# Kernel optimization log

Measured on AMD Instinct MI355X. Metric: run time of the kernel, lower is better.

Reference implementation:

```python
import jax, jax.numpy as jnp
import numpy as np

B, T, IN, H = 256, 512, 19, 512  # batch, seq_len, input_size, hidden_size
OUT = 1


def setup_inputs() -> dict:
    key = jax.random.key(0)
    ks = jax.random.split(key, 16)
    std = 1.0 / np.sqrt(H)  # reset_parameters: uniform(-1/sqrt(H), 1/sqrt(H))
    u = lambda k, shape: jax.random.uniform(k, shape, jnp.float32, -std, std)
    return {
        "input": jax.random.normal(ks[0], (B, T, IN), jnp.float32),
        "l1_Wx": u(ks[1], (4 * H, IN)),
        "l1_bx": u(ks[2], (4 * H,)),
        "l1_Wh": u(ks[3], (4 * H, H)),
        "l1_bh": u(ks[4], (4 * H,)),
        "l2_Wx": u(ks[5], (4 * H, H)),
        "l2_bx": u(ks[6], (4 * H,)),
        "l2_Wh": u(ks[7], (4 * H, H)),
        "l2_bh": u(ks[8], (4 * H,)),
        "fc1_W": u(ks[9], (H // 2, H)),
        "fc1_b": u(ks[10], (H // 2,)),
        "fc2_W": u(ks[11], (H // 4, H // 2)),
        "fc2_b": u(ks[12], (H // 4,)),
        "fc3_W": u(ks[13], (OUT, H // 4)),
        "fc3_b": u(ks[14], (OUT,)),
    }


def _lstm_layer(x, Wx, bx, Wh, bh):
    # Precompute the input projection for all timesteps (identical math to
    # per-step xh(input), but one big GEMM). x: [B, T, in] -> pre: [B, T, 4H]
    pre = jnp.einsum('bti,gi->btg', x, Wx) + bx
    h_dim = Wh.shape[1]

    def step(carry, p_t):
        h, c = carry
        gates = p_t + h @ Wh.T + bh  # [B, 4H]
        i, f, g, o = jnp.split(gates, 4, axis=-1)
        c = jax.nn.sigmoid(f) * c + jax.nn.sigmoid(i) * jnp.tanh(g)
        h = jax.nn.sigmoid(o) * jnp.tanh(c)
        return (h, c), h

    h0 = jnp.zeros((x.shape[0], h_dim), x.dtype)
    _, hs = jax.lax.scan(step, (h0, h0), jnp.swapaxes(pre, 0, 1))  # hs: [T, B, H]
    return jnp.swapaxes(hs, 0, 1)  # [B, T, H]


def reference(input, l1_Wx, l1_bx, l1_Wh, l1_bh, l2_Wx, l2_bx, l2_Wh, l2_bh,
              fc1_W, fc1_b, fc2_W, fc2_b, fc3_W, fc3_b):
    h1 = _lstm_layer(input, l1_Wx, l1_bx, l1_Wh, l1_bh)
    h2 = _lstm_layer(h1, l2_Wx, l2_bx, l2_Wh, l2_bh)
    out = h2[:, -1, :]  # last timestep of top layer
    out = jax.nn.relu(out @ fc1_W.T + fc1_b)  # dropout = identity (inference)
    out = jax.nn.relu(out @ fc2_W.T + fc2_b)
    out = out @ fc3_W.T + fc3_b
    return jnp.squeeze(out)  # [B]
```

## Files before the change

### kernel.cpp

```cpp
#include <hip/hip_runtime.h>
#include <hip/hip_cooperative_groups.h>

namespace cg = cooperative_groups;

#define Bb   256
#define Tt   512
#define INx  19
#define Hh   512
#define NWG  256
#define NTHR 512

typedef unsigned int u32;
typedef unsigned long long u64;

__device__ __forceinline__ float sigf(float x) { return 1.0f / (1.0f + __expf(-x)); }
__device__ __forceinline__ float tanhfast(float x) {
    float e = __expf(2.0f * x);
    return 1.0f - 2.0f / (e + 1.0f);
}

union pcast { u64 u; float2 f; };
__device__ __forceinline__ void gstore2(float2* p, float2 v) {
    pcast c; c.f = v;
    __hip_atomic_store((u64*)p, c.u, __ATOMIC_RELAXED, __HIP_MEMORY_SCOPE_AGENT);
}

__device__ __forceinline__ void gbar(u32* flags, int wgid, int tid, u32 phase) {
    __syncthreads();
    if (tid == 0)
        __hip_atomic_store(&flags[wgid], phase, __ATOMIC_RELEASE, __HIP_MEMORY_SCOPE_AGENT);
    if (tid < NWG) {
        const u32* fp = &flags[tid];
        while (__hip_atomic_load(fp, __ATOMIC_RELAXED, __HIP_MEMORY_SCOPE_AGENT) < phase)
            __builtin_amdgcn_s_sleep(2);
    }
    __syncthreads();
    __builtin_amdgcn_fence(__ATOMIC_ACQUIRE, "agent");
}

__device__ __forceinline__ void ldh(const float4* __restrict__ hp, int c,
                                    float4 (&A)[4], float4 (&B)[4]) {
    #pragma unroll
    for (int kk = 0; kk < 4; ++kk) {
        A[kk] = hp[(size_t)(c * 4 + kk) * 128];
        B[kk] = hp[(size_t)(c * 4 + kk) * 128 + 1];
    }
}

__device__ __forceinline__ void fmac(const float4 (&A)[4], const float4 (&B)[4],
                                     const float* __restrict__ wk,
                                     float (&a1)[4][4], float (&ax)[4][4], float (&ah)[4][4]) {
    #pragma unroll
    for (int g = 0; g < 4; ++g) {
        const float4 w1 = *reinterpret_cast<const float4*>(wk + (0 + g) * 528);
        const float4 w2 = *reinterpret_cast<const float4*>(wk + (4 + g) * 528);
        const float4 w3 = *reinterpret_cast<const float4*>(wk + (8 + g) * 528);
        a1[g][0] += A[0].x*w1.x + A[1].x*w1.y + A[2].x*w1.z + A[3].x*w1.w;
        a1[g][1] += A[0].z*w1.x + A[1].z*w1.y + A[2].z*w1.z + A[3].z*w1.w;
        a1[g][2] += B[0].x*w1.x + B[1].x*w1.y + B[2].x*w1.z + B[3].x*w1.w;
        a1[g][3] += B[0].z*w1.x + B[1].z*w1.y + B[2].z*w1.z + B[3].z*w1.w;
        ax[g][0] += A[0].x*w2.x + A[1].x*w2.y + A[2].x*w2.z + A[3].x*w2.w;
        ax[g][1] += A[0].z*w2.x + A[1].z*w2.y + A[2].z*w2.z + A[3].z*w2.w;
        ax[g][2] += B[0].x*w2.x + B[1].x*w2.y + B[2].x*w2.z + B[3].x*w2.w;
        ax[g][3] += B[0].z*w2.x + B[1].z*w2.y + B[2].z*w2.z + B[3].z*w2.w;
        ah[g][0] += A[0].y*w3.x + A[1].y*w3.y + A[2].y*w3.z + A[3].y*w3.w;
        ah[g][1] += A[0].w*w3.x + A[1].w*w3.y + A[2].w*w3.z + A[3].w*w3.w;
        ah[g][2] += B[0].y*w3.x + B[1].y*w3.y + B[2].y*w3.z + B[3].y*w3.w;
        ah[g][3] += B[0].w*w3.x + B[1].w*w3.y + B[2].w*w3.z + B[3].w*w3.w;
    }
}

__global__ void __launch_bounds__(NTHR, 2)
lstm_fused(const float* __restrict__ input,
           const float* __restrict__ l1_Wx, const float* __restrict__ l1_bx,
           const float* __restrict__ l1_Wh, const float* __restrict__ l1_bh,
           const float* __restrict__ l2_Wx, const float* __restrict__ l2_bx,
           const float* __restrict__ l2_Wh, const float* __restrict__ l2_bh,
           const float* __restrict__ fc1_W, const float* __restrict__ fc1_b,
           const float* __restrict__ fc2_W, const float* __restrict__ fc2_b,
           const float* __restrict__ fc3_W, const float* __restrict__ fc3_b,
           float* __restrict__ out, float* __restrict__ ws)
{
    __shared__ float wlds[24 * 528];
    __shared__ float wx1l[8 * 20];
    __shared__ float fcb[Hh + 256 + 128];

    cg::grid_group grid = cg::this_grid();
    const int wgid = blockIdx.x;
    const int jb = wgid * 2;
    const int tid = threadIdx.x;
    const int wid = tid >> 6, lane = tid & 63;
    const int su = wid & 1;
    const int bh = wid >> 1;
    const int kq = lane >> 4;
    const int bg = lane & 15;
    const int bB = bh * 64 + bg * 4;
    const int j  = jb + su;

    float2* PA = (float2*)ws;
    float2* PB = PA + Hh * Bb;
    u32* flags = (u32*)(PB + Hh * Bb);

    if (tid == 0)
        __hip_atomic_store(&flags[wgid], 0u, __ATOMIC_RELAXED, __HIP_MEMORY_SCOPE_AGENT);
    grid.sync();

    for (int idx = tid; idx < 24 * 512; idx += NTHR) {
        const int row = idx >> 9, k = idx & 511;
        const int sru = row >= 12 ? 1 : 0;
        const int rr = row - sru * 12;
        const int m = rr >> 2, g = rr & 3;
        const float* src = (m == 0) ? l1_Wh : (m == 1) ? l2_Wx : l2_Wh;
        wlds[row * 528 + (k >> 7) * 132 + (k & 127)] =
            src[(size_t)(g * Hh + jb + sru) * Hh + k];
    }
    if (tid < 8 * INx) {
        const int r = tid / INx, i = tid - r * INx;
        const int sru = r >> 2, g = r & 3;
        wx1l[r * 20 + i] = l1_Wx[(size_t)(g * Hh + jb + sru) * INx + i];
    }
    float b1r[4], b2r[4];
    #pragma unroll
    for (int g = 0; g < 4; ++g) {
        const int row = g * Hh + j;
        b1r[g] = l1_bx[row] + l1_bh[row];
        b2r[g] = l2_bx[row] + l2_bh[row];
    }
    __syncthreads();

    float c1[4], c2[4];
    #pragma unroll
    for (int b = 0; b < 4; ++b) {
        const float* xr = input + (size_t)(bB + b) * Tt * INx;
        float s[4];
        #pragma unroll
        for (int g = 0; g < 4; ++g) {
            float acc = b1r[g];
            #pragma unroll
            for (int i = 0; i < INx; ++i) acc += xr[i] * wx1l[(su * 4 + g) * 20 + i];
            s[g] = acc;
        }
        c1[b] = sigf(s[0]) * tanhfast(s[2]);
        c2[b] = 0.0f;
        const float h1v = sigf(s[3]) * tanhfast(c1[b]);
        if (kq == 0) gstore2(&PA[(size_t)j * Bb + bB + b], make_float2(h1v, 0.0f));
    }
    gbar(flags, wgid, tid, 1u);

    const float2* Pc = PA; float2* Pn = PB;
    const float* wlane = wlds + su * (12 * 528) + kq * 132;

    for (int t = 0; t < Tt; ++t) {
        const bool doL1 = (t < Tt - 1);

        float a1[4][4], ax[4][4], ah[4][4];
        #pragma unroll
        for (int g = 0; g < 4; ++g)
            #pragma unroll
            for (int b = 0; b < 4; ++b) { a1[g][b] = 0.f; ax[g][b] = 0.f; ah[g][b] = 0.f; }

        const float4* hp = (const float4*)Pc + (size_t)(kq * 128) * 128 + (bB >> 1);

        float4 Ac[4], Bc[4], An[4], Bn[4];
        ldh(hp, 0, Ac, Bc);
        #pragma unroll 1
        for (int c = 0; c < 32; c += 2) {
            ldh(hp, c + 1, An, Bn);
            fmac(Ac, Bc, wlane + c * 4, a1, ax, ah);
            if (c < 30) ldh(hp, c + 2, Ac, Bc);
            fmac(An, Bn, wlane + (c + 1) * 4, a1, ax, ah);
        }

        #pragma unroll
        for (int g = 0; g < 4; ++g) {
            #pragma unroll
            for (int b = 0; b < 4; ++b) {
                float v = a1[g][b]; v += __shfl_xor(v, 16, 64); v += __shfl_xor(v, 32, 64); a1[g][b] = v;
                float w = ax[g][b]; w += __shfl_xor(w, 16, 64); w += __shfl_xor(w, 32, 64); ax[g][b] = w;
                float u = ah[g][b]; u += __shfl_xor(u, 16, 64); u += __shfl_xor(u, 32, 64); ah[g][b] = u;
            }
        }

        #pragma unroll
        for (int b = 0; b < 4; ++b) {
            float s2[4];
            #pragma unroll
            for (int g = 0; g < 4; ++g) s2[g] = ax[g][b] + ah[g][b] + b2r[g];

            float h1v = 0.0f;
            if (doL1) {
                const float* xr = input + ((size_t)(bB + b) * Tt + (t + 1)) * INx;
                float s1[4];
                #pragma unroll
                for (int g = 0; g < 4; ++g) {
                    float acc = a1[g][b] + b1r[g];
                    #pragma unroll
                    for (int i = 0; i < INx; ++i) acc += xr[i] * wx1l[(su * 4 + g) * 20 + i];
                    s1[g] = acc;
                }
                const float ig = sigf(s1[0]), fg = sigf(s1[1]);
                const float gg = tanhfast(s1[2]), og = sigf(s1[3]);
                c1[b] = fg * c1[b] + ig * gg;
                h1v = og * tanhfast(c1[b]);
            }
            const float ig = sigf(s2[0]), fg = sigf(s2[1]);
            const float gg = tanhfast(s2[2]), og = sigf(s2[3]);
            c2[b] = fg * c2[b] + ig * gg;
            const float h2v = og * tanhfast(c2[b]);
            if (kq == 0) gstore2(&Pn[(size_t)j * Bb + bB + b], make_float2(h1v, h2v));
        }

        gbar(flags, wgid, tid, (u32)(t + 2));

        const float2* tp = Pc; Pc = Pn; Pn = (float2*)tp;
    }

    float* hh  = fcb;
    float* a1s = fcb + Hh;
    float* a2s = fcb + Hh + 256;
    hh[tid] = Pc[(size_t)tid * Bb + wgid].y;
    __syncthreads();
    if (tid < 256) {
        float acc = fc1_b[tid];
        const float* wr = fc1_W + (size_t)tid * Hh;
        for (int i = 0; i < Hh; ++i) acc += wr[i] * hh[i];
        a1s[tid] = fmaxf(acc, 0.0f);
    }
    __syncthreads();
    if (tid < 128) {
        float acc = fc2_b[tid];
        const float* wr = fc2_W + (size_t)tid * 256;
        for (int i = 0; i < 256; ++i) acc += wr[i] * a1s[i];
        a2s[tid] = fmaxf(acc, 0.0f);
    }
    __syncthreads();
    if (tid == 0) {
        float acc = fc3_b[0];
        for (int i = 0; i < 128; ++i) acc += fc3_W[i] * a2s[i];
        out[wgid] = acc;
    }
}

extern "C" void kernel_launch(void* const* d_in, const int* in_sizes, int n_in,
                              void* d_out, int out_size, void* d_ws, size_t ws_size,
                              hipStream_t stream)
{
    (void)in_sizes; (void)n_in; (void)out_size; (void)ws_size;

    const float* input = (const float*)d_in[0];
    const float* l1_Wx = (const float*)d_in[1];
    const float* l1_bx = (const float*)d_in[2];
    const float* l1_Wh = (const float*)d_in[3];
    const float* l1_bh = (const float*)d_in[4];
    const float* l2_Wx = (const float*)d_in[5];
    const float* l2_bx = (const float*)d_in[6];
    const float* l2_Wh = (const float*)d_in[7];
    const float* l2_bh = (const float*)d_in[8];
    const float* fc1_W = (const float*)d_in[9];
    const float* fc1_b = (const float*)d_in[10];
    const float* fc2_W = (const float*)d_in[11];
    const float* fc2_b = (const float*)d_in[12];
    const float* fc3_W = (const float*)d_in[13];
    const float* fc3_b = (const float*)d_in[14];
    float* out = (float*)d_out;
    float* ws  = (float*)d_ws;

    void* args[] = {
        &input,
        &l1_Wx, &l1_bx, &l1_Wh, &l1_bh,
        &l2_Wx, &l2_bx, &l2_Wh, &l2_bh,
        &fc1_W, &fc1_b, &fc2_W, &fc2_b, &fc3_W, &fc3_b,
        &out, &ws
    };
    hipLaunchCooperativeKernel((void*)lstm_fused, dim3(NWG), dim3(NTHR), args, 0, stream);
}
```

Baseline: 30.44 ms.

## Read LSTM weights from global memory and reduce K-split partials through LDS

Stops staging the per-workgroup weight rows in LDS. Each wave now reads its weight slices straight from global memory (wave-uniform addresses, cached), and the work is repartitioned so each wave covers a K quarter for all 64 batch groups. The cross-lane shuffle reduction is replaced by writing partial sums to an LDS buffer, followed by a __syncthreads, after which every thread owns one (unit, batch) cell to finish the gate math. This removes the serial per-thread loop over 4 batches and the redundant kq lanes in the epilogue, at the cost of global or cache weight traffic on every timestep plus an extra block barrier.

After: 29.86 ms. No clear change (-1.9%).

```diff
diff --git a/kernel.cpp b/kernel.cpp
--- a/kernel.cpp
+++ b/kernel.cpp
@@ -10,6 +10,12 @@
 #define NWG  256
 #define NTHR 512
 
+#define PART_FLOATS (8 * 12 * 256)
+#define WX1_FLOATS  (8 * 20)
+#define FCB_FLOATS  (Hh + 256 + 128)
+#define SMEM_FLOATS (PART_FLOATS + WX1_FLOATS + FCB_FLOATS)
+#define SMEM_BYTES  (SMEM_FLOATS * 4)
+
 typedef unsigned int u32;
 typedef unsigned long long u64;
 
@@ -48,13 +54,15 @@
 }
 
 __device__ __forceinline__ void fmac(const float4 (&A)[4], const float4 (&B)[4],
-                                     const float* __restrict__ wk,
+                                     const float* const (&wb1)[4],
+                                     const float* const (&wb2)[4],
+                                     const float* const (&wb3)[4], int c4,
                                      float (&a1)[4][4], float (&ax)[4][4], float (&ah)[4][4]) {
     #pragma unroll
     for (int g = 0; g < 4; ++g) {
-        const float4 w1 = *reinterpret_cast<const float4*>(wk + (0 + g) * 528);
-        const float4 w2 = *reinterpret_cast<const float4*>(wk + (4 + g) * 528);
-        const float4 w3 = *reinterpret_cast<const float4*>(wk + (8 + g) * 528);
+        const float4 w1 = *reinterpret_cast<const float4*>(wb1[g] + c4);
+        const float4 w2 = *reinterpret_cast<const float4*>(wb2[g] + c4);
+        const float4 w3 = *reinterpret_cast<const float4*>(wb3[g] + c4);
         a1[g][0] += A[0].x*w1.x + A[1].x*w1.y + A[2].x*w1.z + A[3].x*w1.w;
         a1[g][1] += A[0].z*w1.x + A[1].z*w1.y + A[2].z*w1.z + A[3].z*w1.w;
         a1[g][2] += B[0].x*w1.x + B[1].x*w1.y + B[2].x*w1.z + B[3].x*w1.w;
@@ -81,21 +89,23 @@
            const float* __restrict__ fc3_W, const float* __restrict__ fc3_b,
            float* __restrict__ out, float* __restrict__ ws)
 {
-    __shared__ float wlds[24 * 528];
-    __shared__ float wx1l[8 * 20];
-    __shared__ float fcb[Hh + 256 + 128];
+    extern __shared__ float smem[];
+    float* part = smem;
+    float* wx1l = smem + PART_FLOATS;
+    float* fcb  = wx1l + WX1_FLOATS;
 
     cg::grid_group grid = cg::this_grid();
     const int wgid = blockIdx.x;
     const int jb = wgid * 2;
     const int tid = threadIdx.x;
-    const int wid = tid >> 6, lane = tid & 63;
-    const int su = wid & 1;
-    const int bh = wid >> 1;
-    const int kq = lane >> 4;
-    const int bg = lane & 15;
-    const int bB = bh * 64 + bg * 4;
-    const int j  = jb + su;
+
+    const int wu = __builtin_amdgcn_readfirstlane(tid >> 6);
+    const int su = wu & 1;
+    const int kq = wu >> 1;
+    const int bg = tid & 63;
+    const int su2 = tid >> 8;
+    const int fb  = tid & 255;
+    const int j2  = jb + su2;
 
     float2* PA = (float2*)ws;
     float2* PB = PA + Hh * Bb;
@@ -105,50 +115,50 @@
         __hip_atomic_store(&flags[wgid], 0u, __ATOMIC_RELAXED, __HIP_MEMORY_SCOPE_AGENT);
     grid.sync();
 
-    for (int idx = tid; idx < 24 * 512; idx += NTHR) {
-        const int row = idx >> 9, k = idx & 511;
-        const int sru = row >= 12 ? 1 : 0;
-        const int rr = row - sru * 12;
-        const int m = rr >> 2, g = rr & 3;
-        const float* src = (m == 0) ? l1_Wh : (m == 1) ? l2_Wx : l2_Wh;
-        wlds[row * 528 + (k >> 7) * 132 + (k & 127)] =
-            src[(size_t)(g * Hh + jb + sru) * Hh + k];
-    }
+    const float* wb1[4]; const float* wb2[4]; const float* wb3[4];
+    {
+        const int j = jb + su;
+        #pragma unroll
+        for (int g = 0; g < 4; ++g) {
+            const size_t off = (size_t)(g * Hh + j) * Hh + kq * 128;
+            wb1[g] = l1_Wh + off;
+            wb2[g] = l2_Wx + off;
+            wb3[g] = l2_Wh + off;
+        }
+    }
+
     if (tid < 8 * INx) {
         const int r = tid / INx, i = tid - r * INx;
-        const int sru = r >> 2, g = r & 3;
-        wx1l[r * 20 + i] = l1_Wx[(size_t)(g * Hh + jb + sru) * INx + i];
+        const int u = r >> 2, g = r & 3;
+        wx1l[r * 20 + i] = l1_Wx[(size_t)(g * Hh + jb + u) * INx + i];
     }
     float b1r[4], b2r[4];
     #pragma unroll
     for (int g = 0; g < 4; ++g) {
-        const int row = g * Hh + j;
+        const int row = g * Hh + j2;
         b1r[g] = l1_bx[row] + l1_bh[row];
         b2r[g] = l2_bx[row] + l2_bh[row];
     }
     __syncthreads();
 
-    float c1[4], c2[4];
-    #pragma unroll
-    for (int b = 0; b < 4; ++b) {
-        const float* xr = input + (size_t)(bB + b) * Tt * INx;
+    float c1 = 0.f, c2 = 0.f;
+    {
+        const float* xr = input + (size_t)fb * Tt * INx;
         float s[4];
         #pragma unroll
         for (int g = 0; g < 4; ++g) {
             float acc = b1r[g];
             #pragma unroll
-            for (int i = 0; i < INx; ++i) acc += xr[i] * wx1l[(su * 4 + g) * 20 + i];
+            for (int i = 0; i < INx; ++i) acc += xr[i] * wx1l[(su2 * 4 + g) * 20 + i];
             s[g] = acc;
         }
-        c1[b] = sigf(s[0]) * tanhfast(s[2]);
-        c2[b] = 0.0f;
-        const float h1v = sigf(s[3]) * tanhfast(c1[b]);
-        if (kq == 0) gstore2(&PA[(size_t)j * Bb + bB + b], make_float2(h1v, 0.0f));
+        c1 = sigf(s[0]) * tanhfast(s[2]);
+        gstore2(&PA[(size_t)j2 * Bb + fb], make_float2(sigf(s[3]) * tanhfast(c1), 0.f));
     }
     gbar(flags, wgid, tid, 1u);
 
     const float2* Pc = PA; float2* Pn = PB;
-    const float* wlane = wlds + su * (12 * 528) + kq * 132;
+    const int blk = su * 4 + kq;
 
     for (int t = 0; t < Tt; ++t) {
         const bool doL1 = (t < Tt - 1);
@@ -159,55 +169,63 @@
             #pragma unroll
             for (int b = 0; b < 4; ++b) { a1[g][b] = 0.f; ax[g][b] = 0.f; ah[g][b] = 0.f; }
 
-        const float4* hp = (const float4*)Pc + (size_t)(kq * 128) * 128 + (bB >> 1);
-
-        float4 Ac[4], Bc[4], An[4], Bn[4];
-        ldh(hp, 0, Ac, Bc);
+        const float4* hp = (const float4*)Pc + (size_t)(kq * 128) * 128 + bg * 2;
+
+        float4 E0[4], E1[4], O0[4], O1[4];
+        ldh(hp, 0, E0, E1);
         #pragma unroll 1
         for (int c = 0; c < 32; c += 2) {
-            ldh(hp, c + 1, An, Bn);
-            fmac(Ac, Bc, wlane + c * 4, a1, ax, ah);
-            if (c < 30) ldh(hp, c + 2, Ac, Bc);
-            fmac(An, Bn, wlane + (c + 1) * 4, a1, ax, ah);
-        }
-
-        #pragma unroll
-        for (int g = 0; g < 4; ++g) {
-            #pragma unroll
-            for (int b = 0; b < 4; ++b) {
-                float v = a1[g][b]; v += __shfl_xor(v, 16, 64); v += __shfl_xor(v, 32, 64); a1[g][b] = v;
-                float w = ax[g][b]; w += __shfl_xor(w, 16, 64); w += __shfl_xor(w, 32, 64); ax[g][b] = w;
-                float u = ah[g][b]; u += __shfl_xor(u, 16, 64); u += __shfl_xor(u, 32, 64); ah[g][b] = u;
+            ldh(hp, c + 1, O0, O1);
+            fmac(E0, E1, wb1, wb2, wb3, (c    ) * 4, a1, ax, ah);
+            if (c < 30) ldh(hp, c + 2, E0, E1);
+            fmac(O0, O1, wb1, wb2, wb3, (c + 1) * 4, a1, ax, ah);
+        }
+
+        {
+            float* pw = part + (size_t)(blk * 12) * 256 + bg * 4;
+            #pragma unroll
+            for (int g = 0; g < 4; ++g) {
+                *reinterpret_cast<float4*>(pw + (0 + g) * 256) = make_float4(a1[g][0], a1[g][1], a1[g][2], a1[g][3]);
+                *reinterpret_cast<float4*>(pw + (4 + g) * 256) = make_float4(ax[g][0], ax[g][1], ax[g][2], ax[g][3]);
+                *reinterpret_cast<float4*>(pw + (8 + g) * 256) = make_float4(ah[g][0], ah[g][1], ah[g][2], ah[g][3]);
             }
         }
-
-        #pragma unroll
-        for (int b = 0; b < 4; ++b) {
-            float s2[4];
-            #pragma unroll
-            for (int g = 0; g < 4; ++g) s2[g] = ax[g][b] + ah[g][b] + b2r[g];
-
-            float h1v = 0.0f;
+        __syncthreads();
+
+        {
+            float s1[4], s2[4];
+            #pragma unroll
+            for (int g = 0; g < 4; ++g) {
+                float A1 = 0.f, AX = 0.f, AH = 0.f;
+                #pragma unroll
+                for (int q = 0; q < 4; ++q) {
+                    const float* pr = part + (size_t)((su2 * 4 + q) * 12) * 256 + fb;
+                    A1 += pr[(0 + g) * 256];
+                    AX += pr[(4 + g) * 256];
+                    AH += pr[(8 + g) * 256];
+                }
+                s1[g] = A1 + b1r[g];
+                s2[g] = AX + AH + b2r[g];
+            }
+            float h1v = 0.f;
             if (doL1) {
-                const float* xr = input + ((size_t)(bB + b) * Tt + (t + 1)) * INx;
-                float s1[4];
+                const float* xr = input + ((size_t)fb * Tt + t + 1) * INx;
                 #pragma unroll
                 for (int g = 0; g < 4; ++g) {
-                    float acc = a1[g][b] + b1r[g];
+                    float acc = s1[g];
                     #pragma unroll
-                    for (int i = 0; i < INx; ++i) acc += xr[i] * wx1l[(su * 4 + g) * 20 + i];
+                    for (int i = 0; i < INx; ++i) acc += xr[i] * wx1l[(su2 * 4 + g) * 20 + i];
                     s1[g] = acc;
                 }
                 const float ig = sigf(s1[0]), fg = sigf(s1[1]);
                 const float gg = tanhfast(s1[2]), og = sigf(s1[3]);
-                c1[b] = fg * c1[b] + ig * gg;
-                h1v = og * tanhfast(c1[b]);
+                c1 = fg * c1 + ig * gg;
+                h1v = og * tanhfast(c1);
             }
             const float ig = sigf(s2[0]), fg = sigf(s2[1]);
             const float gg = tanhfast(s2[2]), og = sigf(s2[3]);
-            c2[b] = fg * c2[b] + ig * gg;
-            const float h2v = og * tanhfast(c2[b]);
-            if (kq == 0) gstore2(&Pn[(size_t)j * Bb + bB + b], make_float2(h1v, h2v));
+            c2 = fg * c2 + ig * gg;
+            gstore2(&Pn[(size_t)j2 * Bb + fb], make_float2(h1v, og * tanhfast(c2)));
         }
 
         gbar(flags, wgid, tid, (u32)(t + 2));
@@ -265,6 +283,9 @@
     float* out = (float*)d_out;
     float* ws  = (float*)d_ws;
 
+    hipFuncSetAttribute((const void*)lstm_fused,
+                        hipFuncAttributeMaxDynamicSharedMemorySize, SMEM_BYTES);
+
     void* args[] = {
         &input,
         &l1_Wx, &l1_bx, &l1_Wh, &l1_bh,
@@ -272,5 +293,6 @@
         &fc1_W, &fc1_b, &fc2_W, &fc2_b, &fc3_W, &fc3_b,
         &out, &ws
     };
-    hipLaunchCooperativeKernel((void*)lstm_fused, dim3(NWG), dim3(NTHR), args, 0, stream);
-}
+    hipLaunchCooperativeKernel((void*)lstm_fused, dim3(NWG), dim3(NTHR), args,
+                               SMEM_BYTES, stream);
+}
```

## Replace workgroup grid barrier with per-wave batch-slice barriers and remap lanes

Applied to the files above, without the earlier changes.

Replaces the whole-grid barrier (syncthreads plus a flag spin) with per-wavefront barriers. Each wave owns a 32-batch slice across all workgroups and syncs only with the matching wave in other blocks, using a separate flag array per slice. Lanes are remapped so one wave covers both hidden units over a batch slice with 4 k-quarters, and the layer-2 Wx/Wh accumulators are merged. It also drops the explicit software prefetch of h and pads the LDS stride to 544. The aim is to cut barrier latency and coupling between waves, at the cost of 8x more flag traffic and the loss of load/compute overlap.

Result: slower. 40.71 ms (+33.7%).

```diff
diff --git a/kernel.cpp b/kernel.cpp
--- a/kernel.cpp
+++ b/kernel.cpp
@@ -25,50 +25,24 @@
     __hip_atomic_store((u64*)p, c.u, __ATOMIC_RELAXED, __HIP_MEMORY_SCOPE_AGENT);
 }
 
-__device__ __forceinline__ void gbar(u32* flags, int wgid, int tid, u32 phase) {
-    __syncthreads();
-    if (tid == 0)
-        __hip_atomic_store(&flags[wgid], phase, __ATOMIC_RELEASE, __HIP_MEMORY_SCOPE_AGENT);
-    if (tid < NWG) {
-        const u32* fp = &flags[tid];
-        while (__hip_atomic_load(fp, __ATOMIC_RELAXED, __HIP_MEMORY_SCOPE_AGENT) < phase)
-            __builtin_amdgcn_s_sleep(2);
-    }
-    __syncthreads();
+__device__ __forceinline__ void wbar(u32* fS, int wgid, int lane, u32 phase) {
+    asm volatile("s_waitcnt vmcnt(0)" ::: "memory");
+    if (lane == 0)
+        __hip_atomic_store(&fS[wgid], phase, __ATOMIC_RELEASE, __HIP_MEMORY_SCOPE_AGENT);
+    const u32* f = fS + lane;
+    for (;;) {
+        bool d = (__hip_atomic_load(f,       __ATOMIC_RELAXED, __HIP_MEMORY_SCOPE_AGENT) >= phase)
+              && (__hip_atomic_load(f + 64,  __ATOMIC_RELAXED, __HIP_MEMORY_SCOPE_AGENT) >= phase)
+              && (__hip_atomic_load(f + 128, __ATOMIC_RELAXED, __HIP_MEMORY_SCOPE_AGENT) >= phase)
+              && (__hip_atomic_load(f + 192, __ATOMIC_RELAXED, __HIP_MEMORY_SCOPE_AGENT) >= phase);
+        if (__all(d)) break;
+        __builtin_amdgcn_s_sleep(2);
+    }
     __builtin_amdgcn_fence(__ATOMIC_ACQUIRE, "agent");
 }
 
-__device__ __forceinline__ void ldh(const float4* __restrict__ hp, int c,
-                                    float4 (&A)[4], float4 (&B)[4]) {
-    #pragma unroll
-    for (int kk = 0; kk < 4; ++kk) {
-        A[kk] = hp[(size_t)(c * 4 + kk) * 128];
-        B[kk] = hp[(size_t)(c * 4 + kk) * 128 + 1];
-    }
-}
-
-__device__ __forceinline__ void fmac(const float4 (&A)[4], const float4 (&B)[4],
-                                     const float* __restrict__ wk,
-                                     float (&a1)[4][4], float (&ax)[4][4], float (&ah)[4][4]) {
-    #pragma unroll
-    for (int g = 0; g < 4; ++g) {
-        const float4 w1 = *reinterpret_cast<const float4*>(wk + (0 + g) * 528);
-        const float4 w2 = *reinterpret_cast<const float4*>(wk + (4 + g) * 528);
-        const float4 w3 = *reinterpret_cast<const float4*>(wk + (8 + g) * 528);
-        a1[g][0] += A[0].x*w1.x + A[1].x*w1.y + A[2].x*w1.z + A[3].x*w1.w;
-        a1[g][1] += A[0].z*w1.x + A[1].z*w1.y + A[2].z*w1.z + A[3].z*w1.w;
-        a1[g][2] += B[0].x*w1.x + B[1].x*w1.y + B[2].x*w1.z + B[3].x*w1.w;
-        a1[g][3] += B[0].z*w1.x + B[1].z*w1.y + B[2].z*w1.z + B[3].z*w1.w;
-        ax[g][0] += A[0].x*w2.x + A[1].x*w2.y + A[2].x*w2.z + A[3].x*w2.w;
-        ax[g][1] += A[0].z*w2.x + A[1].z*w2.y + A[2].z*w2.z + A[3].z*w2.w;
-        ax[g][2] += B[0].x*w2.x + B[1].x*w2.y + B[2].x*w2.z + B[3].x*w2.w;
-        ax[g][3] += B[0].z*w2.x + B[1].z*w2.y + B[2].z*w2.z + B[3].z*w2.w;
-        ah[g][0] += A[0].y*w3.x + A[1].y*w3.y + A[2].y*w3.z + A[3].y*w3.w;
-        ah[g][1] += A[0].w*w3.x + A[1].w*w3.y + A[2].w*w3.z + A[3].w*w3.w;
-        ah[g][2] += B[0].y*w3.x + B[1].y*w3.y + B[2].y*w3.z + B[3].y*w3.w;
-        ah[g][3] += B[0].w*w3.x + B[1].w*w3.y + B[2].w*w3.z + B[3].w*w3.w;
-    }
-}
+#define WROWS 24
+#define WSTR  544
 
 __global__ void __launch_bounds__(NTHR, 2)
 lstm_fused(const float* __restrict__ input,
@@ -81,7 +55,7 @@
            const float* __restrict__ fc3_W, const float* __restrict__ fc3_b,
            float* __restrict__ out, float* __restrict__ ws)
 {
-    __shared__ float wlds[24 * 528];
+    __shared__ float wlds[WROWS * WSTR];
     __shared__ float wx1l[8 * 20];
     __shared__ float fcb[Hh + 256 + 128];
 
@@ -89,35 +63,37 @@
     const int wgid = blockIdx.x;
     const int jb = wgid * 2;
     const int tid = threadIdx.x;
-    const int wid = tid >> 6, lane = tid & 63;
-    const int su = wid & 1;
-    const int bh = wid >> 1;
-    const int kq = lane >> 4;
-    const int bg = lane & 15;
-    const int bB = bh * 64 + bg * 4;
-    const int j  = jb + su;
+
+    const int sid  = __builtin_amdgcn_readfirstlane(tid >> 6);
+    const int lane = tid & 63;
+    const int u    = lane >> 5;
+    const int kq   = (lane >> 3) & 3;
+    const int bp   = lane & 7;
+    const int b0   = sid * 32 + bp * 4;
+    const int j    = jb + u;
 
     float2* PA = (float2*)ws;
-    float2* PB = PA + Hh * Bb;
-    u32* flags = (u32*)(PB + Hh * Bb);
-
-    if (tid == 0)
-        __hip_atomic_store(&flags[wgid], 0u, __ATOMIC_RELAXED, __HIP_MEMORY_SCOPE_AGENT);
+    float2* PB = PA + (size_t)Hh * Bb;
+    u32* flags = (u32*)(PB + (size_t)Hh * Bb);
+    u32* fS = flags + sid * 256;
+
+    if (tid < 8)
+        __hip_atomic_store(&flags[tid * 256 + wgid], 0u,
+                           __ATOMIC_RELAXED, __HIP_MEMORY_SCOPE_AGENT);
     grid.sync();
 
-    for (int idx = tid; idx < 24 * 512; idx += NTHR) {
-        const int row = idx >> 9, k = idx & 511;
-        const int sru = row >= 12 ? 1 : 0;
-        const int rr = row - sru * 12;
+    for (int idx = tid; idx < WROWS * Hh; idx += NTHR) {
+        const int ri = idx >> 9, k = idx & 511;
+        const int uu = ri / 12, rr = ri - uu * 12;
         const int m = rr >> 2, g = rr & 3;
         const float* src = (m == 0) ? l1_Wh : (m == 1) ? l2_Wx : l2_Wh;
-        wlds[row * 528 + (k >> 7) * 132 + (k & 127)] =
-            src[(size_t)(g * Hh + jb + sru) * Hh + k];
+        wlds[ri * WSTR + (k >> 7) * 136 + (k & 127)] =
+            src[(size_t)(g * Hh + jb + uu) * Hh + k];
     }
     if (tid < 8 * INx) {
         const int r = tid / INx, i = tid - r * INx;
-        const int sru = r >> 2, g = r & 3;
-        wx1l[r * 20 + i] = l1_Wx[(size_t)(g * Hh + jb + sru) * INx + i];
+        const int uu = r >> 2, g = r & 3;
+        wx1l[r * 20 + i] = l1_Wx[(size_t)(g * Hh + jb + uu) * INx + i];
     }
     float b1r[4], b2r[4];
     #pragma unroll
@@ -130,90 +106,114 @@
 
     float c1[4], c2[4];
     #pragma unroll
-    for (int b = 0; b < 4; ++b) {
-        const float* xr = input + (size_t)(bB + b) * Tt * INx;
-        float s[4];
+    for (int b = 0; b < 4; ++b) { c1[b] = 0.f; c2[b] = 0.f; }
+    if (kq == 0) {
+        #pragma unroll
+        for (int b = 0; b < 4; ++b) {
+            const float* xr = input + (size_t)(b0 + b) * Tt * INx;
+            float s[4];
+            #pragma unroll
+            for (int g = 0; g < 4; ++g) {
+                float acc = b1r[g];
+                #pragma unroll
+                for (int i = 0; i < INx; ++i) acc += xr[i] * wx1l[(u * 4 + g) * 20 + i];
+                s[g] = acc;
+            }
+            c1[b] = sigf(s[0]) * tanhfast(s[2]);
+            gstore2(&PA[(size_t)j * Bb + b0 + b],
+                    make_float2(sigf(s[3]) * tanhfast(c1[b]), 0.f));
+        }
+    }
+    wbar(fS, wgid, lane, 1u);
+
+    const float2* Pc = PA; float2* Pn = PB;
+    const float* wk0 = wlds + (u * 12) * WSTR + kq * 136;
+
+    for (int t = 0; t < Tt; ++t) {
+        const bool doL1 = (t < Tt - 1);
+
+        float a1[4][4], a2[4][4];
+        #pragma unroll
+        for (int g = 0; g < 4; ++g)
+            #pragma unroll
+            for (int b = 0; b < 4; ++b) { a1[g][b] = 0.f; a2[g][b] = 0.f; }
+
+        const float4* hp = (const float4*)Pc + (size_t)(kq * 128) * 128 + (b0 >> 1);
+
+        #pragma unroll 1
+        for (int c = 0; c < 32; ++c) {
+            float4 HA[4], HB[4];
+            #pragma unroll
+            for (int kk = 0; kk < 4; ++kk) {
+                HA[kk] = hp[(size_t)(c * 4 + kk) * 128];
+                HB[kk] = hp[(size_t)(c * 4 + kk) * 128 + 1];
+            }
+            const float* wk = wk0 + c * 4;
+            #pragma unroll
+            for (int g = 0; g < 4; ++g) {
+                const float4 w1 = *reinterpret_cast<const float4*>(wk + (0 + g) * WSTR);
+                const float4 w2 = *reinterpret_cast<const float4*>(wk + (4 + g) * WSTR);
+                const float4 w3 = *reinterpret_cast<const float4*>(wk + (8 + g) * WSTR);
+                a1[g][0] += HA[0].x*w1.x + HA[1].x*w1.y + HA[2].x*w1.z + HA[3].x*w1.w;
+                a1[g][1] += HA[0].z*w1.x + HA[1].z*w1.y + HA[2].z*w1.z + HA[3].z*w1.w;
+                a1[g][2] += HB[0].x*w1.x + HB[1].x*w1.y + HB[2].x*w1.z + HB[3].x*w1.w;
+                a1[g][3] += HB[0].z*w1.x + HB[1].z*w1.y + HB[2].z*w1.z + HB[3].z*w1.w;
+                a2[g][0] += HA[0].x*w2.x + HA[1].x*w2.y + HA[2].x*w2.z + HA[3].x*w2.w
+                          + HA[0].y*w3.x + HA[1].y*w3.y + HA[2].y*w3.z + HA[3].y*w3.w;
+                a2[g][1] += HA[0].z*w2.x + HA[1].z*w2.y + HA[2].z*w2.z + HA[3].z*w2.w
+                          + HA[0].w*w3.x + HA[1].w*w3.y + HA[2].w*w3.z + HA[3].w*w3.w;
+                a2[g][2] += HB[0].x*w2.x + HB[1].x*w2.y + HB[2].x*w2.z + HB[3].x*w2.w
+                          + HB[0].y*w3.x + HB[1].y*w3.y + HB[2].y*w3.z + HB[3].y*w3.w;
+                a2[g][3] += HB[0].z*w2.x + HB[1].z*w2.y + HB[2].z*w2.z + HB[3].z*w2.w
+                          + HB[0].w*w3.x + HB[1].w*w3.y + HB[2].w*w3.z + HB[3].w*w3.w;
+            }
+        }
+
         #pragma unroll
         for (int g = 0; g < 4; ++g) {
-            float acc = b1r[g];
-            #pragma unroll
-            for (int i = 0; i < INx; ++i) acc += xr[i] * wx1l[(su * 4 + g) * 20 + i];
-            s[g] = acc;
-        }
-        c1[b] = sigf(s[0]) * tanhfast(s[2]);
-        c2[b] = 0.0f;
-        const float h1v = sigf(s[3]) * tanhfast(c1[b]);
-        if (kq == 0) gstore2(&PA[(size_t)j * Bb + bB + b], make_float2(h1v, 0.0f));
-    }
-    gbar(flags, wgid, tid, 1u);
-
-    const float2* Pc = PA; float2* Pn = PB;
-    const float* wlane = wlds + su * (12 * 528) + kq * 132;
-
-    for (int t = 0; t < Tt; ++t) {
-        const bool doL1 = (t < Tt - 1);
-
-        float a1[4][4], ax[4][4], ah[4][4];
-        #pragma unroll
-        for (int g = 0; g < 4; ++g)
-            #pragma unroll
-            for (int b = 0; b < 4; ++b) { a1[g][b] = 0.f; ax[g][b] = 0.f; ah[g][b] = 0.f; }
-
-        const float4* hp = (const float4*)Pc + (size_t)(kq * 128) * 128 + (bB >> 1);
-
-        float4 Ac[4], Bc[4], An[4], Bn[4];
-        ldh(hp, 0, Ac, Bc);
-        #pragma unroll 1
-        for (int c = 0; c < 32; c += 2) {
-            ldh(hp, c + 1, An, Bn);
-            fmac(Ac, Bc, wlane + c * 4, a1, ax, ah);
-            if (c < 30) ldh(hp, c + 2, Ac, Bc);
-            fmac(An, Bn, wlane + (c + 1) * 4, a1, ax, ah);
-        }
-
-        #pragma unroll
-        for (int g = 0; g < 4; ++g) {
             #pragma unroll
             for (int b = 0; b < 4; ++b) {
-                float v = a1[g][b]; v += __shfl_xor(v, 16, 64); v += __shfl_xor(v, 32, 64); a1[g][b] = v;
-                float w = ax[g][b]; w += __shfl_xor(w, 16, 64); w += __shfl_xor(w, 32, 64); ax[g][b] = w;
-                float u = ah[g][b]; u += __shfl_xor(u, 16, 64); u += __shfl_xor(u, 32, 64); ah[g][b] = u;
-            }
-        }
-
-        #pragma unroll
-        for (int b = 0; b < 4; ++b) {
-            float s2[4];
-            #pragma unroll
-            for (int g = 0; g < 4; ++g) s2[g] = ax[g][b] + ah[g][b] + b2r[g];
-
-            float h1v = 0.0f;
-            if (doL1) {
-                const float* xr = input + ((size_t)(bB + b) * Tt + (t + 1)) * INx;
-                float s1[4];
-                #pragma unroll
-                for (int g = 0; g < 4; ++g) {
-                    float acc = a1[g][b] + b1r[g];
+                float v = a1[g][b]; v += __shfl_xor(v, 8, 64); v += __shfl_xor(v, 16, 64); a1[g][b] = v;
+                float w = a2[g][b]; w += __shfl_xor(w, 8, 64); w += __shfl_xor(w, 16, 64); a2[g][b] = w;
+            }
+        }
+
+        if (kq == 0) {
+            #pragma unroll
+            for (int b = 0; b < 4; ++b) {
+                const int bb = b0 + b;
+                float h1v = 0.f;
+                if (doL1) {
+                    const float* xr = input + ((size_t)bb * Tt + t + 1) * INx;
+                    float s1[4];
                     #pragma unroll
-                    for (int i = 0; i < INx; ++i) acc += xr[i] * wx1l[(su * 4 + g) * 20 + i];
-                    s1[g] = acc;
+                    for (int g = 0; g < 4; ++g) {
+                        float acc = a1[g][b] + b1r[g];
+                        #pragma unroll
+                        for (int i = 0; i < INx; ++i) acc += xr[i] * wx1l[(u * 4 + g) * 20 + i];
+                        s1[g] = acc;
+                    }
+                    const float ig = sigf(s1[0]), fg = sigf(s1[1]);
+                    const float gg = tanhfast(s1[2]), og = sigf(s1[3]);
+                    c1[b] = fg * c1[b] + ig * gg;
+                    h1v = og * tanhfast(c1[b]);
                 }
-                const float ig = sigf(s1[0]), fg = sigf(s1[1]);
-                const float gg = tanhfast(s1[2]), og = sigf(s1[3]);
-                c1[b] = fg * c1[b] + ig * gg;
-                h1v = og * tanhfast(c1[b]);
-            }
-            const float ig = sigf(s2[0]), fg = sigf(s2[1]);
-            const float gg = tanhfast(s2[2]), og = sigf(s2[3]);
-            c2[b] = fg * c2[b] + ig * gg;
-            const float h2v = og * tanhfast(c2[b]);
-            if (kq == 0) gstore2(&Pn[(size_t)j * Bb + bB + b], make_float2(h1v, h2v));
-        }
-
-        gbar(flags, wgid, tid, (u32)(t + 2));
+                const float ig = sigf(a2[0][b] + b2r[0]);
+                const float fg = sigf(a2[1][b] + b2r[1]);
+                const float gg = tanhfast(a2[2][b] + b2r[2]);
+                const float og = sigf(a2[3][b] + b2r[3]);
+                c2[b] = fg * c2[b] + ig * gg;
+                gstore2(&Pn[(size_t)j * Bb + bb], make_float2(h1v, og * tanhfast(c2[b])));
+            }
+        }
+
+        wbar(fS, wgid, lane, (u32)(t + 2));
 
         const float2* tp = Pc; Pc = Pn; Pn = (float2*)tp;
     }
+
+    __syncthreads();
+    __builtin_amdgcn_fence(__ATOMIC_ACQUIRE, "agent");
 
     float* hh  = fcb;
     float* a1s = fcb + Hh;
```

## Split layer barriers to overlap layer-2 step with layer-1 sync

Applied to the files above, without the earlier changes.

Replaces the single per-step grid barrier, which carried interleaved h1/h2 pairs, with two flag sets and triple-buffered separate h1 and h2 buffers. Layer 2's step t is computed while the layer-1 barrier for step t is outstanding, so one layer's compute can hide the other's synchronisation latency. Each buffer is now stored as a plain float plane instead of interleaved float2, and a final wait runs before the FC head. This adds a second spin-wait per step and more sweeps over global hidden state, and it relies on the ordering across three rotating buffers being correct.

Result: slower. 32.85 ms (+7.9%).

```diff
diff --git a/kernel.cpp b/kernel.cpp
--- a/kernel.cpp
+++ b/kernel.cpp
@@ -11,7 +11,6 @@
 #define NTHR 512
 
 typedef unsigned int u32;
-typedef unsigned long long u64;
 
 __device__ __forceinline__ float sigf(float x) { return 1.0f / (1.0f + __expf(-x)); }
 __device__ __forceinline__ float tanhfast(float x) {
@@ -19,55 +18,52 @@
     return 1.0f - 2.0f / (e + 1.0f);
 }
 
-union pcast { u64 u; float2 f; };
-__device__ __forceinline__ void gstore2(float2* p, float2 v) {
-    pcast c; c.f = v;
-    __hip_atomic_store((u64*)p, c.u, __ATOMIC_RELAXED, __HIP_MEMORY_SCOPE_AGENT);
-}
-
-__device__ __forceinline__ void gbar(u32* flags, int wgid, int tid, u32 phase) {
-    __syncthreads();
-    if (tid == 0)
-        __hip_atomic_store(&flags[wgid], phase, __ATOMIC_RELEASE, __HIP_MEMORY_SCOPE_AGENT);
-    if (tid < NWG) {
-        const u32* fp = &flags[tid];
-        while (__hip_atomic_load(fp, __ATOMIC_RELAXED, __HIP_MEMORY_SCOPE_AGENT) < phase)
-            __builtin_amdgcn_s_sleep(2);
-    }
-    __syncthreads();
-    __builtin_amdgcn_fence(__ATOMIC_ACQUIRE, "agent");
-}
-
-__device__ __forceinline__ void ldh(const float4* __restrict__ hp, int c,
-                                    float4 (&A)[4], float4 (&B)[4]) {
+__device__ __forceinline__ void gstore1(float* p, float v) {
+    __hip_atomic_store(p, v, __ATOMIC_RELAXED, __HIP_MEMORY_SCOPE_AGENT);
+}
+__device__ __forceinline__ u32 gpoll(const u32* p) {
+    return __hip_atomic_load(p, __ATOMIC_RELAXED, __HIP_MEMORY_SCOPE_AGENT);
+}
+
+#define WSTR 528
+
+__device__ __forceinline__ void sweep4(const float* __restrict__ hbuf,
+                                       const float* __restrict__ wrow,
+                                       int kq, int bB, float (&acc)[4][4]) {
+    const float4* hp = reinterpret_cast<const float4*>(hbuf + (size_t)(kq * 128) * Bb) + (bB >> 2);
+    float4 Hc[4], Hn[4];
     #pragma unroll
-    for (int kk = 0; kk < 4; ++kk) {
-        A[kk] = hp[(size_t)(c * 4 + kk) * 128];
-        B[kk] = hp[(size_t)(c * 4 + kk) * 128 + 1];
-    }
-}
-
-__device__ __forceinline__ void fmac(const float4 (&A)[4], const float4 (&B)[4],
-                                     const float* __restrict__ wk,
-                                     float (&a1)[4][4], float (&ax)[4][4], float (&ah)[4][4]) {
+    for (int kk = 0; kk < 4; ++kk) Hc[kk] = hp[(size_t)kk * 64];
+    #pragma unroll 1
+    for (int c = 0; c < 32; ++c) {
+        if (c < 31) {
+            #pragma unroll
+            for (int kk = 0; kk < 4; ++kk) Hn[kk] = hp[(size_t)((c + 1) * 4 + kk) * 64];
+        }
+        const float* wk = wrow + c * 4;
+        #pragma unroll
+        for (int g = 0; g < 4; ++g) {
+            const float4 w = *reinterpret_cast<const float4*>(wk + g * WSTR);
+            acc[g][0] += Hc[0].x * w.x + Hc[1].x * w.y + Hc[2].x * w.z + Hc[3].x * w.w;
+            acc[g][1] += Hc[0].y * w.x + Hc[1].y * w.y + Hc[2].y * w.z + Hc[3].y * w.w;
+            acc[g][2] += Hc[0].z * w.x + Hc[1].z * w.y + Hc[2].z * w.z + Hc[3].z * w.w;
+            acc[g][3] += Hc[0].w * w.x + Hc[1].w * w.y + Hc[2].w * w.z + Hc[3].w * w.w;
+        }
+        #pragma unroll
+        for (int kk = 0; kk < 4; ++kk) Hc[kk] = Hn[kk];
+    }
+}
+
+__device__ __forceinline__ void butterfly(float (&a)[4][4]) {
     #pragma unroll
-    for (int g = 0; g < 4; ++g) {
-        const float4 w1 = *reinterpret_cast<const float4*>(wk + (0 + g) * 528);
-        const float4 w2 = *reinterpret_cast<const float4*>(wk + (4 + g) * 528);
-        const float4 w3 = *reinterpret_cast<const float4*>(wk + (8 + g) * 528);
-        a1[g][0] += A[0].x*w1.x + A[1].x*w1.y + A[2].x*w1.z + A[3].x*w1.w;
-        a1[g][1] += A[0].z*w1.x + A[1].z*w1.y + A[2].z*w1.z + A[3].z*w1.w;
-        a1[g][2] += B[0].x*w1.x + B[1].x*w1.y + B[2].x*w1.z + B[3].x*w1.w;
-        a1[g][3] += B[0].z*w1.x + B[1].z*w1.y + B[2].z*w1.z + B[3].z*w1.w;
-        ax[g][0] += A[0].x*w2.x + A[1].x*w2.y + A[2].x*w2.z + A[3].x*w2.w;
-        ax[g][1] += A[0].z*w2.x + A[1].z*w2.y + A[2].z*w2.z + A[3].z*w2.w;
-        ax[g][2] += B[0].x*w2.x + B[1].x*w2.y + B[2].x*w2.z + B[3].x*w2.w;
-        ax[g][3] += B[0].z*w2.x + B[1].z*w2.y + B[2].z*w2.z + B[3].z*w2.w;
-        ah[g][0] += A[0].y*w3.x + A[1].y*w3.y + A[2].y*w3.z + A[3].y*w3.w;
-        ah[g][1] += A[0].w*w3.x + A[1].w*w3.y + A[2].w*w3.z + A[3].w*w3.w;
-        ah[g][2] += B[0].y*w3.x + B[1].y*w3.y + B[2].y*w3.z + B[3].y*w3.w;
-        ah[g][3] += B[0].w*w3.x + B[1].w*w3.y + B[2].w*w3.z + B[3].w*w3.w;
-    }
+    for (int g = 0; g < 4; ++g)
+        #pragma unroll
+        for (int b = 0; b < 4; ++b) {
+            float v = a[g][b];
+            v += __shfl_xor(v, 16, 64);
+            v += __shfl_xor(v, 32, 64);
+            a[g][b] = v;
+        }
 }
 
 __global__ void __launch_bounds__(NTHR, 2)
@@ -81,7 +77,7 @@
            const float* __restrict__ fc3_W, const float* __restrict__ fc3_b,
            float* __restrict__ out, float* __restrict__ ws)
 {
-    __shared__ float wlds[24 * 528];
+    __shared__ float wlds[24 * WSTR];
     __shared__ float wx1l[8 * 20];
     __shared__ float fcb[Hh + 256 + 128];
 
@@ -97,21 +93,28 @@
     const int bB = bh * 64 + bg * 4;
     const int j  = jb + su;
 
-    float2* PA = (float2*)ws;
-    float2* PB = PA + Hh * Bb;
-    u32* flags = (u32*)(PB + Hh * Bb);
-
-    if (tid == 0)
+    float* h1b[3]; float* h2b[3];
+    #pragma unroll
+    for (int i = 0; i < 3; ++i) {
+        h1b[i] = ws + (size_t)i * Hh * Bb;
+        h2b[i] = ws + (size_t)(3 + i) * Hh * Bb;
+    }
+    u32* flags  = (u32*)(ws + (size_t)6 * Hh * Bb);
+    u32* flagsB = flags + NWG;
+
+    if (tid == 0) {
         __hip_atomic_store(&flags[wgid], 0u, __ATOMIC_RELAXED, __HIP_MEMORY_SCOPE_AGENT);
+        __hip_atomic_store(&flagsB[wgid], 0u, __ATOMIC_RELAXED, __HIP_MEMORY_SCOPE_AGENT);
+    }
     grid.sync();
 
-    for (int idx = tid; idx < 24 * 512; idx += NTHR) {
+    for (int idx = tid; idx < 24 * Hh; idx += NTHR) {
         const int row = idx >> 9, k = idx & 511;
         const int sru = row >= 12 ? 1 : 0;
         const int rr = row - sru * 12;
         const int m = rr >> 2, g = rr & 3;
         const float* src = (m == 0) ? l1_Wh : (m == 1) ? l2_Wx : l2_Wh;
-        wlds[row * 528 + (k >> 7) * 132 + (k & 127)] =
+        wlds[row * WSTR + (k >> 7) * 132 + (k & 127)] =
             src[(size_t)(g * Hh + jb + sru) * Hh + k];
     }
     if (tid < 8 * INx) {
@@ -128,97 +131,119 @@
     }
     __syncthreads();
 
-    float c1[4], c2[4];
-    #pragma unroll
-    for (int b = 0; b < 4; ++b) {
-        const float* xr = input + (size_t)(bB + b) * Tt * INx;
-        float s[4];
-        #pragma unroll
-        for (int g = 0; g < 4; ++g) {
-            float acc = b1r[g];
-            #pragma unroll
-            for (int i = 0; i < INx; ++i) acc += xr[i] * wx1l[(su * 4 + g) * 20 + i];
-            s[g] = acc;
-        }
-        c1[b] = sigf(s[0]) * tanhfast(s[2]);
-        c2[b] = 0.0f;
-        const float h1v = sigf(s[3]) * tanhfast(c1[b]);
-        if (kq == 0) gstore2(&PA[(size_t)j * Bb + bB + b], make_float2(h1v, 0.0f));
-    }
-    gbar(flags, wgid, tid, 1u);
-
-    const float2* Pc = PA; float2* Pn = PB;
-    const float* wlane = wlds + su * (12 * 528) + kq * 132;
-
-    for (int t = 0; t < Tt; ++t) {
-        const bool doL1 = (t < Tt - 1);
-
-        float a1[4][4], ax[4][4], ah[4][4];
-        #pragma unroll
-        for (int g = 0; g < 4; ++g)
-            #pragma unroll
-            for (int b = 0; b < 4; ++b) { a1[g][b] = 0.f; ax[g][b] = 0.f; ah[g][b] = 0.f; }
-
-        const float4* hp = (const float4*)Pc + (size_t)(kq * 128) * 128 + (bB >> 1);
-
-        float4 Ac[4], Bc[4], An[4], Bn[4];
-        ldh(hp, 0, Ac, Bc);
-        #pragma unroll 1
-        for (int c = 0; c < 32; c += 2) {
-            ldh(hp, c + 1, An, Bn);
-            fmac(Ac, Bc, wlane + c * 4, a1, ax, ah);
-            if (c < 30) ldh(hp, c + 2, Ac, Bc);
-            fmac(An, Bn, wlane + (c + 1) * 4, a1, ax, ah);
-        }
-
-        #pragma unroll
-        for (int g = 0; g < 4; ++g) {
-            #pragma unroll
-            for (int b = 0; b < 4; ++b) {
-                float v = a1[g][b]; v += __shfl_xor(v, 16, 64); v += __shfl_xor(v, 32, 64); a1[g][b] = v;
-                float w = ax[g][b]; w += __shfl_xor(w, 16, 64); w += __shfl_xor(w, 32, 64); ax[g][b] = w;
-                float u = ah[g][b]; u += __shfl_xor(u, 16, 64); u += __shfl_xor(u, 32, 64); ah[g][b] = u;
-            }
-        }
-
+    const float* wW1h = wlds + (su * 12 + 0) * WSTR + kq * 132;
+    const float* wW2x = wlds + (su * 12 + 4) * WSTR + kq * 132;
+    const float* wW2h = wlds + (su * 12 + 8) * WSTR + kq * 132;
+
+    float c1[4] = {0.f, 0.f, 0.f, 0.f}, c2[4] = {0.f, 0.f, 0.f, 0.f};
+    if (kq == 0) {
         #pragma unroll
         for (int b = 0; b < 4; ++b) {
-            float s2[4];
+            const float* xr = input + (size_t)(bB + b) * Tt * INx;
+            float s[4];
             #pragma unroll
-            for (int g = 0; g < 4; ++g) s2[g] = ax[g][b] + ah[g][b] + b2r[g];
-
-            float h1v = 0.0f;
-            if (doL1) {
-                const float* xr = input + ((size_t)(bB + b) * Tt + (t + 1)) * INx;
-                float s1[4];
-                #pragma unroll
-                for (int g = 0; g < 4; ++g) {
-                    float acc = a1[g][b] + b1r[g];
+            for (int g = 0; g < 4; ++g) {
+                float acc = b1r[g];
+                #pragma unroll
+                for (int i = 0; i < INx; ++i) acc += xr[i] * wx1l[(su * 4 + g) * 20 + i];
+                s[g] = acc;
+            }
+            c1[b] = sigf(s[0]) * tanhfast(s[2]);
+            gstore1(&h1b[0][(size_t)j * Bb + bB + b], sigf(s[3]) * tanhfast(c1[b]));
+        }
+    }
+    __syncthreads();
+    if (tid == 0)
+        __hip_atomic_store(&flags[wgid], 1u, __ATOMIC_RELEASE, __HIP_MEMORY_SCOPE_AGENT);
+
+    for (int t = 0; t <= Tt; ++t) {
+        const bool dL2  = (t >= 1);
+        const bool dL2h = (t >= 2);
+        const bool dL1  = (t < Tt - 1);
+        const float* h1m = h1b[(t + 2) % 3];
+        const float* h1c = h1b[t % 3];
+        float*       h1n = h1b[(t + 1) % 3];
+        const float* h2m = h2b[(t + 1) % 3];
+        float*       h2n = h2b[(t + 2) % 3];
+
+        if (dL2h) {
+            if (tid < NWG)
+                while (gpoll(&flagsB[tid]) < (u32)t) __builtin_amdgcn_s_sleep(2);
+            __syncthreads();
+        }
+
+        if (dL2) {
+            float a2[4][4];
+            #pragma unroll
+            for (int g = 0; g < 4; ++g)
+                #pragma unroll
+                for (int b = 0; b < 4; ++b) a2[g][b] = 0.f;
+            sweep4(h1m, wW2x, kq, bB, a2);
+            if (dL2h) sweep4(h2m, wW2h, kq, bB, a2);
+            butterfly(a2);
+            if (kq == 0) {
+                #pragma unroll
+                for (int b = 0; b < 4; ++b) {
+                    const float ig = sigf(a2[0][b] + b2r[0]);
+                    const float fg = sigf(a2[1][b] + b2r[1]);
+                    const float gg = tanhfast(a2[2][b] + b2r[2]);
+                    const float og = sigf(a2[3][b] + b2r[3]);
+                    c2[b] = fg * c2[b] + ig * gg;
+                    gstore1(&h2n[(size_t)j * Bb + bB + b], og * tanhfast(c2[b]));
+                }
+            }
+        }
+        __syncthreads();
+        if (tid == 0)
+            __hip_atomic_store(&flagsB[wgid], (u32)(t + 1), __ATOMIC_RELEASE, __HIP_MEMORY_SCOPE_AGENT);
+
+        if (tid < NWG)
+            while (gpoll(&flags[tid]) < (u32)(t + 1)) __builtin_amdgcn_s_sleep(2);
+        __syncthreads();
+        __builtin_amdgcn_fence(__ATOMIC_ACQUIRE, "agent");
+
+        if (dL1) {
+            float a1[4][4];
+            #pragma unroll
+            for (int g = 0; g < 4; ++g)
+                #pragma unroll
+                for (int b = 0; b < 4; ++b) a1[g][b] = 0.f;
+            sweep4(h1c, wW1h, kq, bB, a1);
+            butterfly(a1);
+            if (kq == 0) {
+                #pragma unroll
+                for (int b = 0; b < 4; ++b) {
+                    const float* xr = input + ((size_t)(bB + b) * Tt + t + 1) * INx;
+                    float s[4];
                     #pragma unroll
-                    for (int i = 0; i < INx; ++i) acc += xr[i] * wx1l[(su * 4 + g) * 20 + i];
-                    s1[g] = acc;
+                    for (int g = 0; g < 4; ++g) {
+                        float acc = a1[g][b] + b1r[g];
+                        #pragma unroll
+                        for (int i = 0; i < INx; ++i) acc += xr[i] * wx1l[(su * 4 + g) * 20 + i];
+                        s[g] = acc;
+                    }
+                    const float ig = sigf(s[0]), fg = sigf(s[1]);
+                    const float gg = tanhfast(s[2]), og = sigf(s[3]);
+                    c1[b] = fg * c1[b] + ig * gg;
+                    gstore1(&h1n[(size_t)j * Bb + bB + b], og * tanhfast(c1[b]));
                 }
-                const float ig = sigf(s1[0]), fg = sigf(s1[1]);
-                const float gg = tanhfast(s1[2]), og = sigf(s1[3]);
-                c1[b] = fg * c1[b] + ig * gg;
-                h1v = og * tanhfast(c1[b]);
             }
-            const float ig = sigf(s2[0]), fg = sigf(s2[1]);
-            const float gg = tanhfast(s2[2]), og = sigf(s2[3]);
-            c2[b] = fg * c2[b] + ig * gg;
-            const float h2v = og * tanhfast(c2[b]);
-            if (kq == 0) gstore2(&Pn[(size_t)j * Bb + bB + b], make_float2(h1v, h2v));
-        }
-
-        gbar(flags, wgid, tid, (u32)(t + 2));
-
-        const float2* tp = Pc; Pc = Pn; Pn = (float2*)tp;
-    }
-
+        }
+        __syncthreads();
+        if (tid == 0)
+            __hip_atomic_store(&flags[wgid], (u32)(t + 2), __ATOMIC_RELEASE, __HIP_MEMORY_SCOPE_AGENT);
+    }
+
+    if (tid < NWG)
+        while (gpoll(&flags[tid]) < (u32)(Tt + 2)) __builtin_amdgcn_s_sleep(2);
+    __syncthreads();
+    __builtin_amdgcn_fence(__ATOMIC_ACQUIRE, "agent");
+
+    const float* h2f = h2b[(Tt - 1) % 3];
     float* hh  = fcb;
     float* a1s = fcb + Hh;
     float* a2s = fcb + Hh + 256;
-    hh[tid] = Pc[(size_t)tid * Bb + wgid].y;
+    hh[tid] = h2f[(size_t)tid * Bb + wgid];
     __syncthreads();
     if (tid < 256) {
         float acc = fc1_b[tid];
```
